# Kernel optimization log

Measured on AMD Instinct MI355X. Metric: run time of the kernel, lower is better.

Reference implementation:

```python
import jax, jax.numpy as jnp
import numpy as np

N_EMBD = 1024
N_HEAD = 16
HEAD_SIZE = N_EMBD // N_HEAD  # 64
B, T = 4, 2048

def setup_inputs() -> dict:
    key = jax.random.key(0)
    k1, k2, k3, k4 = jax.random.split(key, 4)
    x = jax.random.normal(k1, (B, T, N_EMBD), dtype=jnp.float32)
    # weights stored as [in, out]; torch Linear does x @ W.T with W [out,in]
    w_qkv = jax.random.normal(k2, (N_EMBD, 3 * N_EMBD), dtype=jnp.float32) * (N_EMBD ** -0.5)
    w_proj = jax.random.normal(k3, (N_EMBD, N_EMBD), dtype=jnp.float32) * (N_EMBD ** -0.5)
    b_proj = jax.random.normal(k4, (N_EMBD,), dtype=jnp.float32) * 0.01
    return {"x": x, "w_qkv": w_qkv, "w_proj": w_proj, "b_proj": b_proj}

def reference(x, w_qkv, w_proj, b_proj):
    Bx, Tx, C = x.shape
    H, D = N_HEAD, HEAD_SIZE
    qkv = x @ w_qkv                               # [B,T,3C]
    q, k, v = jnp.split(qkv, 3, axis=-1)
    q = q.reshape(Bx, Tx, H, D).transpose(0, 2, 1, 3)  # [B,H,T,D]
    k = k.reshape(Bx, Tx, H, D).transpose(0, 2, 1, 3)
    v = v.reshape(Bx, Tx, H, D).transpose(0, 2, 1, 3)
    att = jnp.einsum('bhqd,bhkd->bhqk', q, k) * (D ** -0.5)  # [B,H,T,T]
    causal = jnp.tril(jnp.ones((Tx, Tx), dtype=bool))
    att = jnp.where(causal[None, None], att, -jnp.inf)
    att = jax.nn.softmax(att, axis=-1)
    out = jnp.einsum('bhqk,bhkd->bhqd', att, v)   # [B,H,T,D]
    out = out.transpose(0, 2, 1, 3).reshape(Bx, Tx, H * D)
    return out @ w_proj + b_proj
```

## Files before the change

kernel.cpp:

```cpp
#include <hip/hip_runtime.h>
#include <hip/hip_bf16.h>
#include <stdint.h>
#include <math.h>


typedef __attribute__((ext_vector_type(8))) short short8;
typedef __attribute__((ext_vector_type(4))) short shrt4;
typedef __attribute__((ext_vector_type(4))) float f32x4;

#define LOG2E 1.44269504088896340736f
#define QSCALE 0.18033688011112042f

__device__ int g_isf32;

__device__ __forceinline__ void gl16(const void* g, void* l) {
  __builtin_amdgcn_global_load_lds(
      (const __attribute__((address_space(1))) unsigned int*)g,
      (__attribute__((address_space(3))) unsigned int*)l, 16, 0, 0);
}

__device__ __forceinline__ short f2bf(float f) {
  __hip_bfloat16 h = __float2bfloat16(f);
  return *reinterpret_cast<short*>(&h);
}
__device__ __forceinline__ float bf2f(short s) {
  __hip_bfloat16 h = *reinterpret_cast<__hip_bfloat16*>(&s);
  return __bfloat162float(h);
}
__device__ __forceinline__ short8 pack8(f32x4 lo, f32x4 hi) {
  short8 r;
#pragma unroll
  for (int e = 0; e < 4; ++e) { r[e] = f2bf(lo[e]); r[4 + e] = f2bf(hi[e]); }
  return r;
}

__device__ __forceinline__ short pbf(float f) {
  unsigned u = __builtin_bit_cast(unsigned, f);
  return (short)((u + 0x8000u) >> 16);
}

__device__ __forceinline__ float dpp_max16(float x) {
  int i;
  i = __builtin_amdgcn_update_dpp(0, __builtin_bit_cast(int, x), 0xB1, 0xF, 0xF, true);
  x = fmaxf(x, __builtin_bit_cast(float, i));
  i = __builtin_amdgcn_update_dpp(0, __builtin_bit_cast(int, x), 0x4E, 0xF, 0xF, true);
  x = fmaxf(x, __builtin_bit_cast(float, i));
  i = __builtin_amdgcn_update_dpp(0, __builtin_bit_cast(int, x), 0x141, 0xF, 0xF, true);
  x = fmaxf(x, __builtin_bit_cast(float, i));
  i = __builtin_amdgcn_update_dpp(0, __builtin_bit_cast(int, x), 0x140, 0xF, 0xF, true);
  x = fmaxf(x, __builtin_bit_cast(float, i));
  return x;
}
__device__ __forceinline__ float dpp_sum16(float x) {
  int i;
  i = __builtin_amdgcn_update_dpp(0, __builtin_bit_cast(int, x), 0xB1, 0xF, 0xF, true);
  x += __builtin_bit_cast(float, i);
  i = __builtin_amdgcn_update_dpp(0, __builtin_bit_cast(int, x), 0x4E, 0xF, 0xF, true);
  x += __builtin_bit_cast(float, i);
  i = __builtin_amdgcn_update_dpp(0, __builtin_bit_cast(int, x), 0x141, 0xF, 0xF, true);
  x += __builtin_bit_cast(float, i);
  i = __builtin_amdgcn_update_dpp(0, __builtin_bit_cast(int, x), 0x140, 0xF, 0xF, true);
  x += __builtin_bit_cast(float, i);
  return x;
}

__global__ __launch_bounds__(256) void detect_dtype(const unsigned short* w) {
  __shared__ int cnt;
  if (threadIdx.x == 0) cnt = 0;
  __syncthreads();
  const unsigned short* p = w + (long)blockIdx.x * 49152;
  int c = 0;
  for (int i = threadIdx.x; i < 49152; i += 256)
    if (((p[i] >> 7) & 0xFF) == 0xFF) c++;
  atomicAdd(&cnt, c);
  __syncthreads();
  if (threadIdx.x == 0) g_isf32 = (cnt > 8) ? 1 : 0;
}

__global__ __launch_bounds__(256) void cvt_x(const void* __restrict__ src,
                                             short* __restrict__ dst) {
  const long i = ((long)blockIdx.x * 256 + threadIdx.x) * 8;
  if (g_isf32) {
    const float* s = (const float*)src + i;
    *(short8*)(dst + i) = pack8(*(const f32x4*)s, *(const f32x4*)(s + 4));
  } else {
    *(short8*)(dst + i) = *(const short8*)((const short*)src + i);
  }
}

template <int MODE>
__global__ __launch_bounds__(512, 2) void gemm_bt(
    const short* __restrict__ A, const short* __restrict__ Bt,
    const void* __restrict__ bias, void* __restrict__ C,
    short* __restrict__ vt, int M, int N, int K)
{
  __shared__ __align__(16) short As[3][16384];
  __shared__ __align__(16) short Bs[3][8192];
  const int tid  = threadIdx.x;
  const int lane = tid & 63;
  const int wave = tid >> 6;
  const int quad = lane >> 4;
  const int l16  = lane & 15;
  const int wm = (wave >> 1) * 64;
  const int wn = (wave & 1) * 64;

  const int gx = (int)gridDim.x;
  const int nwg = gx * (int)gridDim.y;
  int lb = (int)blockIdx.y * gx + (int)blockIdx.x;
  if ((nwg & 7) == 0) lb = (lb & 7) * (nwg >> 3) + (lb >> 3);
  const long m0 = (long)(lb / gx) * 256;
  const long n0 = (long)(lb % gx) * 128;

  int isf32 = 0;
  if (MODE == 1) {
    isf32 = g_isf32;
    asm volatile("s_waitcnt vmcnt(0) lgkmcnt(0)" ::: "memory");
  }

  f32x4 acc[4][4] = {};

  const int srow = tid >> 3;
  const int scol = ((tid & 7) ^ (srow & 7)) * 8;
  const short* Ag = A  + (m0 + srow) * (long)K + scol;
  const short* Bg = Bt + (n0 + srow) * (long)K + scol;
  const long rs64 = (long)64 * K;

  const int x7  = l16 & 7;
  const int xo0 = ((0 + quad) ^ x7) * 16;
  const int xo1 = ((4 + quad) ^ x7) * 16;
  const int aRow = (wm + l16) * 128;
  const int bRow = (wn + l16) * 128;

  auto STAGE_HALF = [&](int t2, int h) {
    const int bb = t2 % 3;
    const long k0 = (long)t2 << 6;
    gl16(Ag + k0 + (h * 2 + 0) * rs64, (char*)As[bb] + (h * 2 + 0) * 8192 + tid * 16);
    gl16(Ag + k0 + (h * 2 + 1) * rs64, (char*)As[bb] + (h * 2 + 1) * 8192 + tid * 16);
    gl16(Bg + k0 + h * rs64,           (char*)Bs[bb] + h * 8192 + tid * 16);
  };

  const int nt = K >> 6;
  STAGE_HALF(0, 0); STAGE_HALF(0, 1);
  STAGE_HALF(1, 0); STAGE_HALF(1, 1);

  for (int t = 0; t < nt; ++t) {
    if (t + 1 < nt) { asm volatile("s_waitcnt vmcnt(6)" ::: "memory"); }
    else            { asm volatile("s_waitcnt vmcnt(0)" ::: "memory"); }
    __builtin_amdgcn_sched_barrier(0);
    __builtin_amdgcn_s_barrier();
    __builtin_amdgcn_sched_barrier(0);

    const char* Ab = (const char*)As[t % 3];
    const char* Bb = (const char*)Bs[t % 3];

#pragma unroll
    for (int ph = 0; ph < 2; ++ph) {
      const int xo = ph ? xo1 : xo0;
      short8 af[4], bfv[4];
#pragma unroll
      for (int i = 0; i < 4; ++i)
        af[i] = *(const short8*)(Ab + aRow + i * 2048 + xo);
#pragma unroll
      for (int j = 0; j < 4; ++j)
        bfv[j] = *(const short8*)(Bb + bRow + j * 2048 + xo);
      if (t + 2 < nt) STAGE_HALF(t + 2, ph);
      __builtin_amdgcn_s_setprio(1);
#pragma unroll
      for (int i = 0; i < 4; ++i)
#pragma unroll
        for (int j = 0; j < 4; ++j)
          acc[i][j] = __builtin_amdgcn_mfma_f32_16x16x32_bf16(af[i], bfv[j], acc[i][j], 0, 0, 0);
      __builtin_amdgcn_s_setprio(0);
      if (ph == 0) {
        __builtin_amdgcn_s_barrier();
        __builtin_amdgcn_sched_barrier(0);
      }
    }
  }

#pragma unroll
  for (int j = 0; j < 4; ++j) {
    const long col = n0 + wn + j * 16 + l16;
    float bv = 0.f;
    if (MODE == 1)
      bv = isf32 ? ((const float*)bias)[col] : bf2f(((const short*)bias)[col]);
#pragma unroll
    for (int i = 0; i < 4; ++i) {
      const long row0 = m0 + wm + i * 16 + quad * 4;
      if (MODE == 2 && col >= 2048) {
        const long bb = row0 >> 11, t0 = row0 & 2047;
        const long hd = col - 2048;
        shrt4 v4;
#pragma unroll
        for (int r = 0; r < 4; ++r) v4[r] = f2bf(acc[i][j][r]);
        *(shrt4*)&vt[((bb * 16 + (hd >> 6)) * 64 + (hd & 63)) * 2048 + t0] = v4;
      } else {
#pragma unroll
        for (int r = 0; r < 4; ++r) {
          const long row = row0 + r;
          const float val = acc[i][j][r] + bv;
          if (MODE == 2) {
            const float vq = (col < 1024) ? val * QSCALE : val;
            ((short*)C)[row * 2048 + col] = f2bf(vq);
          } else {
            if (isf32) ((float*)C)[row * (long)N + col] = val;
            else       ((short*)C)[row * (long)N + col] = f2bf(val);
          }
        }
      }
    }
  }
}

__global__ __launch_bounds__(256) void transpose64(
    const void* __restrict__ src, short* __restrict__ dst, int R, int C)
{
  __shared__ __align__(16) short tile[64][72];
  const int isf32 = g_isf32;
  const int tid = threadIdx.x;
  const long r0 = (long)blockIdx.y * 64;
  const long c0 = (long)blockIdx.x * 64;
#pragma unroll
  for (int it = 0; it < 2; ++it) {
    int idx = it * 256 + tid;
    int rr = idx >> 3, ch = idx & 7;
    const long off = (r0 + rr) * C + c0 + ch * 8;
    short8 v;
    if (isf32) {
      const float* s = (const float*)src + off;
      v = pack8(*(const f32x4*)s, *(const f32x4*)(s + 4));
    } else {
      v = *(const short8*)((const short*)src + off);
    }
    *(short8*)&tile[rr][ch * 8] = v;
  }
  __syncthreads();
#pragma unroll
  for (int it = 0; it < 2; ++it) {
    int idx = it * 256 + tid;
    int cc = idx >> 3, ch = idx & 7;
    short8 v;
#pragma unroll
    for (int jj = 0; jj < 8; ++jj) v[jj] = tile[ch * 8 + jj][cc];
    *(short8*)&dst[(c0 + cc) * R + r0 + ch * 8] = v;
  }
}

__global__ __launch_bounds__(256) void attn_fwd(
    const short* __restrict__ qk, const short* __restrict__ vt,
    short* __restrict__ out)
{
  __shared__ __align__(16) short Ks[2][64][32];
  __shared__ __align__(16) short Vs[2][64][32];
  __shared__ __align__(16) short Pw[4][16][76];
  const int tid = threadIdx.x;
  const int lane = tid & 63, wave = tid >> 6;
  const int quad = lane >> 4, l16 = lane & 15;
  const int bh = blockIdx.x;
  const int b = bh >> 4, h = bh & 15;
  const int jq = (int)gridDim.y - 1 - (int)blockIdx.y;
  const int qbase = jq * 64 + wave * 16;

  const short* qp = qk + ((long)(b * 2048 + qbase + l16)) * 2048 + h * 64 + quad * 8;
  const short8 aq0 = *(const short8*)qp;
  const short8 aq1 = *(const short8*)(qp + 32);

  const int sr = tid >> 2, sc_ = tid & 3;
  const short* kg = qk + (long)b * 2048 * 2048 + 1024 + h * 64 + (long)sr * 2048 + sc_ * 8;
  const short* vg = vt + ((long)bh * 64 + sr) * 2048 + sc_ * 8;

  f32x4 o[4] = {};
  float m_run[4], l_run[4];
#pragma unroll
  for (int r = 0; r < 4; ++r) { m_run[r] = -1e30f; l_run[r] = 0.f; }

  for (int kt = 0; kt < jq; ++kt) {
    const int k0 = kt * 64;

    __syncthreads();
    gl16(kg + (long)k0 * 2048,      (char*)Ks + tid * 16);
    gl16(kg + (long)k0 * 2048 + 32, (char*)Ks + 4096 + tid * 16);
    gl16(vg + k0,                   (char*)Vs + tid * 16);
    gl16(vg + k0 + 32,              (char*)Vs + 4096 + tid * 16);
    __syncthreads();

    f32x4 s[4];
#pragma unroll
    for (int c = 0; c < 4; ++c) {
      short8 kf0 = *(const short8*)&Ks[0][c * 16 + l16][quad * 8];
      short8 kf1 = *(const short8*)&Ks[1][c * 16 + l16][quad * 8];
      f32x4 z = {};
      z = __builtin_amdgcn_mfma_f32_16x16x32_bf16(aq0, kf0, z, 0, 0, 0);
      z = __builtin_amdgcn_mfma_f32_16x16x32_bf16(aq1, kf1, z, 0, 0, 0);
      s[c] = z;
    }

    float mx[4];
#pragma unroll
    for (int r = 0; r < 4; ++r)
      mx[r] = dpp_max16(fmaxf(fmaxf(s[0][r], s[1][r]), fmaxf(s[2][r], s[3][r])));

    int grow = 0;
#pragma unroll
    for (int r = 0; r < 4; ++r) grow |= (mx[r] > m_run[r] + 8.f);
    if (__any(grow)) {
#pragma unroll
      for (int r = 0; r < 4; ++r) {
        const float mn = fmaxf(m_run[r], mx[r]);
        const float al = __builtin_amdgcn_exp2f(m_run[r] - mn);
        m_run[r] = mn;
        l_run[r] *= al;
#pragma unroll
        for (int i = 0; i < 4; ++i) o[i][r] *= al;
      }
    }

#pragma unroll
    for (int c = 0; c < 4; ++c)
#pragma unroll
      for (int r = 0; r < 4; ++r) {
        const float p = __builtin_amdgcn_exp2f(s[c][r] - m_run[r]);
        l_run[r] += p;
        Pw[wave][quad * 4 + r][c * 16 + l16] = pbf(p);
      }

    {
      short8 pf0 = *(const short8*)&Pw[wave][l16][quad * 8];
      short8 pf1 = *(const short8*)&Pw[wave][l16][32 + quad * 8];
#pragma unroll
      for (int i = 0; i < 4; ++i) {
        short8 vf0 = *(const short8*)&Vs[0][i * 16 + l16][quad * 8];
        o[i] = __builtin_amdgcn_mfma_f32_16x16x32_bf16(pf0, vf0, o[i], 0, 0, 0);
        short8 vf1 = *(const short8*)&Vs[1][i * 16 + l16][quad * 8];
        o[i] = __builtin_amdgcn_mfma_f32_16x16x32_bf16(pf1, vf1, o[i], 0, 0, 0);
      }
    }
  }

  {
    const int k0 = jq * 64;

    __syncthreads();
    gl16(kg + (long)k0 * 2048,      (char*)Ks + tid * 16);
    gl16(kg + (long)k0 * 2048 + 32, (char*)Ks + 4096 + tid * 16);
    gl16(vg + k0,                   (char*)Vs + tid * 16);
    gl16(vg + k0 + 32,              (char*)Vs + 4096 + tid * 16);
    __syncthreads();

    f32x4 s[4];
    float mx[4];
#pragma unroll
    for (int r = 0; r < 4; ++r) mx[r] = -1e30f;
#pragma unroll
    for (int c = 0; c < 4; ++c) {
      if (c > wave) continue;
      short8 kf0 = *(const short8*)&Ks[0][c * 16 + l16][quad * 8];
      short8 kf1 = *(const short8*)&Ks[1][c * 16 + l16][quad * 8];
      f32x4 z = {};
      z = __builtin_amdgcn_mfma_f32_16x16x32_bf16(aq0, kf0, z, 0, 0, 0);
      z = __builtin_amdgcn_mfma_f32_16x16x32_bf16(aq1, kf1, z, 0, 0, 0);
      if (c == wave) {
#pragma unroll
        for (int r = 0; r < 4; ++r)
          z[r] = (l16 > quad * 4 + r) ? -1e30f : z[r];
      }
      s[c] = z;
#pragma unroll
      for (int r = 0; r < 4; ++r) mx[r] = fmaxf(mx[r], z[r]);
    }
#pragma unroll
    for (int r = 0; r < 4; ++r) mx[r] = dpp_max16(mx[r]);

    int grow = 0;
#pragma unroll
    for (int r = 0; r < 4; ++r) grow |= (mx[r] > m_run[r] + 8.f);
    if (__any(grow)) {
#pragma unroll
      for (int r = 0; r < 4; ++r) {
        const float mn = fmaxf(m_run[r], mx[r]);
        const float al = __builtin_amdgcn_exp2f(m_run[r] - mn);
        m_run[r] = mn;
        l_run[r] *= al;
#pragma unroll
        for (int i = 0; i < 4; ++i) o[i][r] *= al;
      }
    }

#pragma unroll
    for (int c = 0; c < 4; ++c) {
      if (c <= wave) {
#pragma unroll
        for (int r = 0; r < 4; ++r) {
          const float p = __builtin_amdgcn_exp2f(s[c][r] - m_run[r]);
          l_run[r] += p;
          Pw[wave][quad * 4 + r][c * 16 + l16] = pbf(p);
        }
      } else if (c < 2 || wave >= 2) {
#pragma unroll
        for (int r = 0; r < 4; ++r)
          Pw[wave][quad * 4 + r][c * 16 + l16] = 0;
      }
    }

    {
      short8 pf0 = *(const short8*)&Pw[wave][l16][quad * 8];
#pragma unroll
      for (int i = 0; i < 4; ++i) {
        short8 vf0 = *(const short8*)&Vs[0][i * 16 + l16][quad * 8];
        o[i] = __builtin_amdgcn_mfma_f32_16x16x32_bf16(pf0, vf0, o[i], 0, 0, 0);
      }
      if (wave >= 2) {
        short8 pf1 = *(const short8*)&Pw[wave][l16][32 + quad * 8];
#pragma unroll
        for (int i = 0; i < 4; ++i) {
          short8 vf1 = *(const short8*)&Vs[1][i * 16 + l16][quad * 8];
          o[i] = __builtin_amdgcn_mfma_f32_16x16x32_bf16(pf1, vf1, o[i], 0, 0, 0);
        }
      }
    }
  }

#pragma unroll
  for (int r = 0; r < 4; ++r) l_run[r] = dpp_sum16(l_run[r]);
  float inv[4];
#pragma unroll
  for (int r = 0; r < 4; ++r) inv[r] = 1.0f / l_run[r];
  short* op = out + ((long)(b * 2048 + qbase + quad * 4)) * 1024 + h * 64;
#pragma unroll
  for (int i = 0; i < 4; ++i)
#pragma unroll
    for (int r = 0; r < 4; ++r)
      op[(long)r * 1024 + i * 16 + l16] = f2bf(o[i][r] * inv[r]);
}

__global__ __launch_bounds__(256) void copy_out(const void* __restrict__ src,
                                                void* __restrict__ dst)
{
  const long n16 = g_isf32 ? 2097152L : 1048576L;
  const uint4* s = (const uint4*)src;
  uint4* d = (uint4*)dst;
  for (long i = (long)blockIdx.x * 256 + threadIdx.x; i < n16;
       i += (long)gridDim.x * 256)
    d[i] = s[i];
}

extern "C" void kernel_launch(void* const* d_in, const int* in_sizes, int n_in,
                              void* d_out, int out_size, void* d_ws, size_t ws_size,
                              hipStream_t stream)
{
  const void* x      = d_in[0];
  const void* w_qkv  = d_in[1];
  const void* w_proj = d_in[2];
  const void* b_proj = d_in[3];

  short* ws = (short*)d_ws;
  const bool planA = ws_size >= 67108864ULL;

  short* qk  = ws;
  short* vtp = ws + 16777216L;

  short *wqkvT, *attnb, *wprojT, *xbf;
  void*  projC;
  if (planA) {
    attnb  = ws + 25165824L;
    wqkvT  = attnb;
    wprojT = qk;
    xbf    = (short*)d_out;
    projC  = d_out;
  } else {
    wqkvT  = (short*)d_out;
    xbf    = (short*)d_out + 3145728L;
    attnb  = (short*)d_out;
    wprojT = vtp;
    projC  = qk;
  }

  detect_dtype<<<64, 256, 0, stream>>>((const unsigned short*)w_qkv);
  cvt_x<<<4096, 256, 0, stream>>>(x, xbf);
  transpose64<<<dim3(3072 / 64, 1024 / 64), 256, 0, stream>>>(w_qkv, wqkvT, 1024, 3072);
  gemm_bt<2><<<dim3(3072 / 128, 8192 / 256), 512, 0, stream>>>(
      xbf, wqkvT, nullptr, qk, vtp, 8192, 3072, 1024);
  attn_fwd<<<dim3(64, 32), 256, 0, stream>>>(qk, vtp, attnb);
  transpose64<<<dim3(1024 / 64, 1024 / 64), 256, 0, stream>>>(w_proj, wprojT, 1024, 1024);
  gemm_bt<1><<<dim3(1024 / 128, 8192 / 256), 512, 0, stream>>>(
      attnb, wprojT, b_proj, projC, nullptr, 8192, 1024, 1024);
  if (!planA)
    copy_out<<<2048, 256, 0, stream>>>(projC, d_out);
}
```

Before: 286.4 us.

## Pair causal query tiles per attention block and pack P and V stores with cvt_pk_bf16

```diff
diff --git a/kernel.cpp b/kernel.cpp
--- a/kernel.cpp
+++ b/kernel.cpp
@@ -5,7 +5,6 @@
 
 
 typedef __attribute__((ext_vector_type(8))) short short8;
-typedef __attribute__((ext_vector_type(4))) short shrt4;
 typedef __attribute__((ext_vector_type(4))) float f32x4;
 
 #define LOG2E 1.44269504088896340736f
@@ -34,9 +33,10 @@
   return r;
 }
 
-__device__ __forceinline__ short pbf(float f) {
-  unsigned u = __builtin_bit_cast(unsigned, f);
-  return (short)((u + 0x8000u) >> 16);
+__device__ __forceinline__ unsigned cvtpk(float a, float b) {
+  unsigned r;
+  asm("v_cvt_pk_bf16_f32 %0, %1, %2" : "=v"(r) : "v"(a), "v"(b));
+  return r;
 }
 
 __device__ __forceinline__ float dpp_max16(float x) {
@@ -181,20 +181,24 @@
 #pragma unroll
   for (int j = 0; j < 4; ++j) {
     const long col = n0 + wn + j * 16 + l16;
-    float bv = 0.f;
-    if (MODE == 1)
-      bv = isf32 ? ((const float*)bias)[col] : bf2f(((const short*)bias)[col]);
-#pragma unroll
-    for (int i = 0; i < 4; ++i) {
-      const long row0 = m0 + wm + i * 16 + quad * 4;
-      if (MODE == 2 && col >= 2048) {
-        const long bb = row0 >> 11, t0 = row0 & 2047;
-        const long hd = col - 2048;
-        shrt4 v4;
-#pragma unroll
-        for (int r = 0; r < 4; ++r) v4[r] = f2bf(acc[i][j][r]);
-        *(shrt4*)&vt[((bb * 16 + (hd >> 6)) * 64 + (hd & 63)) * 2048 + t0] = v4;
-      } else {
+    if (MODE == 2 && col >= 2048) {
+      const long hd = col - 2048;
+      const long bb = (m0 + wm) >> 11;
+      const long tb = (m0 + wm) & 2047;
+      short* vrow = vt + ((bb * 16 + (hd >> 6)) * 64 + (hd & 63)) * 2048 + tb;
+#pragma unroll
+      for (int ip = 0; ip < 2; ++ip)
+#pragma unroll
+        for (int r = 0; r < 4; ++r)
+          *(unsigned*)&vrow[ip * 32 + 2 * (quad * 4 + r)] =
+              cvtpk(acc[2 * ip][j][r], acc[2 * ip + 1][j][r]);
+    } else {
+      float bv = 0.f;
+      if (MODE == 1)
+        bv = isf32 ? ((const float*)bias)[col] : bf2f(((const short*)bias)[col]);
+#pragma unroll
+      for (int i = 0; i < 4; ++i) {
+        const long row0 = m0 + wm + i * 16 + quad * 4;
 #pragma unroll
         for (int r = 0; r < 4; ++r) {
           const long row = row0 + r;
@@ -252,185 +256,197 @@
 {
   __shared__ __align__(16) short Ks[2][64][32];
   __shared__ __align__(16) short Vs[2][64][32];
-  __shared__ __align__(16) short Pw[4][16][76];
+  __shared__ __align__(16) unsigned Pw[4][16][36];
   const int tid = threadIdx.x;
   const int lane = tid & 63, wave = tid >> 6;
   const int quad = lane >> 4, l16 = lane & 15;
   const int bh = blockIdx.x;
   const int b = bh >> 4, h = bh & 15;
-  const int jq = (int)gridDim.y - 1 - (int)blockIdx.y;
-  const int qbase = jq * 64 + wave * 16;
-
-  const short* qp = qk + ((long)(b * 2048 + qbase + l16)) * 2048 + h * 64 + quad * 8;
-  const short8 aq0 = *(const short8*)qp;
-  const short8 aq1 = *(const short8*)(qp + 32);
+  const int py = blockIdx.y;
 
   const int sr = tid >> 2, sc_ = tid & 3;
   const short* kg = qk + (long)b * 2048 * 2048 + 1024 + h * 64 + (long)sr * 2048 + sc_ * 8;
   const short* vg = vt + ((long)bh * 64 + sr) * 2048 + sc_ * 8;
 
-  f32x4 o[4] = {};
-  float m_run[4], l_run[4];
-#pragma unroll
-  for (int r = 0; r < 4; ++r) { m_run[r] = -1e30f; l_run[r] = 0.f; }
-
-  for (int kt = 0; kt < jq; ++kt) {
-    const int k0 = kt * 64;
-
-    __syncthreads();
-    gl16(kg + (long)k0 * 2048,      (char*)Ks + tid * 16);
-    gl16(kg + (long)k0 * 2048 + 32, (char*)Ks + 4096 + tid * 16);
-    gl16(vg + k0,                   (char*)Vs + tid * 16);
-    gl16(vg + k0 + 32,              (char*)Vs + 4096 + tid * 16);
-    __syncthreads();
-
-    f32x4 s[4];
-#pragma unroll
-    for (int c = 0; c < 4; ++c) {
-      short8 kf0 = *(const short8*)&Ks[0][c * 16 + l16][quad * 8];
-      short8 kf1 = *(const short8*)&Ks[1][c * 16 + l16][quad * 8];
-      f32x4 z = {};
-      z = __builtin_amdgcn_mfma_f32_16x16x32_bf16(aq0, kf0, z, 0, 0, 0);
-      z = __builtin_amdgcn_mfma_f32_16x16x32_bf16(aq1, kf1, z, 0, 0, 0);
-      s[c] = z;
-    }
-
-    float mx[4];
-#pragma unroll
-    for (int r = 0; r < 4; ++r)
-      mx[r] = dpp_max16(fmaxf(fmaxf(s[0][r], s[1][r]), fmaxf(s[2][r], s[3][r])));
-
-    int grow = 0;
-#pragma unroll
-    for (int r = 0; r < 4; ++r) grow |= (mx[r] > m_run[r] + 8.f);
-    if (__any(grow)) {
+  for (int hseg = 0; hseg < 2; ++hseg) {
+    const int jq = hseg ? (31 - py) : py;
+    const int qbase = jq * 64 + wave * 16;
+
+    const short* qp = qk + ((long)(b * 2048 + qbase + l16)) * 2048 + h * 64 + quad * 8;
+    const short8 aq0 = *(const short8*)qp;
+    const short8 aq1 = *(const short8*)(qp + 32);
+
+    f32x4 o[4] = {};
+    float m_run[4], l_run[4];
+#pragma unroll
+    for (int r = 0; r < 4; ++r) { m_run[r] = -1e30f; l_run[r] = 0.f; }
+
+    for (int kt = 0; kt < jq; ++kt) {
+      const int k0 = kt * 64;
+
+      __syncthreads();
+      gl16(kg + (long)k0 * 2048,      (char*)Ks + tid * 16);
+      gl16(kg + (long)k0 * 2048 + 32, (char*)Ks + 4096 + tid * 16);
+      gl16(vg + k0,                   (char*)Vs + tid * 16);
+      gl16(vg + k0 + 32,              (char*)Vs + 4096 + tid * 16);
+      __syncthreads();
+
+      f32x4 s[4];
+#pragma unroll
+      for (int c = 0; c < 4; ++c) {
+        short8 kf0 = *(const short8*)&Ks[0][c * 16 + l16][quad * 8];
+        short8 kf1 = *(const short8*)&Ks[1][c * 16 + l16][quad * 8];
+        f32x4 z = {};
+        z = __builtin_amdgcn_mfma_f32_16x16x32_bf16(aq0, kf0, z, 0, 0, 0);
+        z = __builtin_amdgcn_mfma_f32_16x16x32_bf16(aq1, kf1, z, 0, 0, 0);
+        s[c] = z;
+      }
+
+      float mx[4];
+#pragma unroll
+      for (int r = 0; r < 4; ++r)
+        mx[r] = dpp_max16(fmaxf(fmaxf(s[0][r], s[1][r]), fmaxf(s[2][r], s[3][r])));
+
+      int grow = 0;
+#pragma unroll
+      for (int r = 0; r < 4; ++r) grow |= (mx[r] > m_run[r] + 8.f);
+      if (__any(grow)) {
+#pragma unroll
+        for (int r = 0; r < 4; ++r) {
+          const float mn = fmaxf(m_run[r], mx[r]);
+          const float al = __builtin_amdgcn_exp2f(m_run[r] - mn);
+          m_run[r] = mn;
+          l_run[r] *= al;
+#pragma unroll
+          for (int i = 0; i < 4; ++i) o[i][r] *= al;
+        }
+      }
+
+      float p[4][4];
+#pragma unroll
+      for (int c = 0; c < 4; ++c)
+#pragma unroll
+        for (int r = 0; r < 4; ++r) {
+          p[c][r] = __builtin_amdgcn_exp2f(s[c][r] - m_run[r]);
+          l_run[r] += p[c][r];
+        }
 #pragma unroll
       for (int r = 0; r < 4; ++r) {
-        const float mn = fmaxf(m_run[r], mx[r]);
-        const float al = __builtin_amdgcn_exp2f(m_run[r] - mn);
-        m_run[r] = mn;
-        l_run[r] *= al;
-#pragma unroll
-        for (int i = 0; i < 4; ++i) o[i][r] *= al;
-      }
-    }
-
-#pragma unroll
-    for (int c = 0; c < 4; ++c)
-#pragma unroll
-      for (int r = 0; r < 4; ++r) {
-        const float p = __builtin_amdgcn_exp2f(s[c][r] - m_run[r]);
-        l_run[r] += p;
-        Pw[wave][quad * 4 + r][c * 16 + l16] = pbf(p);
-      }
-
-    {
-      short8 pf0 = *(const short8*)&Pw[wave][l16][quad * 8];
-      short8 pf1 = *(const short8*)&Pw[wave][l16][32 + quad * 8];
-#pragma unroll
-      for (int i = 0; i < 4; ++i) {
-        short8 vf0 = *(const short8*)&Vs[0][i * 16 + l16][quad * 8];
-        o[i] = __builtin_amdgcn_mfma_f32_16x16x32_bf16(pf0, vf0, o[i], 0, 0, 0);
-        short8 vf1 = *(const short8*)&Vs[1][i * 16 + l16][quad * 8];
-        o[i] = __builtin_amdgcn_mfma_f32_16x16x32_bf16(pf1, vf1, o[i], 0, 0, 0);
-      }
-    }
-  }
-
-  {
-    const int k0 = jq * 64;
-
-    __syncthreads();
-    gl16(kg + (long)k0 * 2048,      (char*)Ks + tid * 16);
-    gl16(kg + (long)k0 * 2048 + 32, (char*)Ks + 4096 + tid * 16);
-    gl16(vg + k0,                   (char*)Vs + tid * 16);
-    gl16(vg + k0 + 32,              (char*)Vs + 4096 + tid * 16);
-    __syncthreads();
-
-    f32x4 s[4];
-    float mx[4];
-#pragma unroll
-    for (int r = 0; r < 4; ++r) mx[r] = -1e30f;
-#pragma unroll
-    for (int c = 0; c < 4; ++c) {
-      if (c > wave) continue;
-      short8 kf0 = *(const short8*)&Ks[0][c * 16 + l16][quad * 8];
-      short8 kf1 = *(const short8*)&Ks[1][c * 16 + l16][quad * 8];
-      f32x4 z = {};
-      z = __builtin_amdgcn_mfma_f32_16x16x32_bf16(aq0, kf0, z, 0, 0, 0);
-      z = __builtin_amdgcn_mfma_f32_16x16x32_bf16(aq1, kf1, z, 0, 0, 0);
-      if (c == wave) {
-#pragma unroll
-        for (int r = 0; r < 4; ++r)
-          z[r] = (l16 > quad * 4 + r) ? -1e30f : z[r];
-      }
-      s[c] = z;
-#pragma unroll
-      for (int r = 0; r < 4; ++r) mx[r] = fmaxf(mx[r], z[r]);
-    }
-#pragma unroll
-    for (int r = 0; r < 4; ++r) mx[r] = dpp_max16(mx[r]);
-
-    int grow = 0;
-#pragma unroll
-    for (int r = 0; r < 4; ++r) grow |= (mx[r] > m_run[r] + 8.f);
-    if (__any(grow)) {
-#pragma unroll
-      for (int r = 0; r < 4; ++r) {
-        const float mn = fmaxf(m_run[r], mx[r]);
-        const float al = __builtin_amdgcn_exp2f(m_run[r] - mn);
-        m_run[r] = mn;
-        l_run[r] *= al;
-#pragma unroll
-        for (int i = 0; i < 4; ++i) o[i][r] *= al;
-      }
-    }
-
-#pragma unroll
-    for (int c = 0; c < 4; ++c) {
-      if (c <= wave) {
-#pragma unroll
-        for (int r = 0; r < 4; ++r) {
-          const float p = __builtin_amdgcn_exp2f(s[c][r] - m_run[r]);
-          l_run[r] += p;
-          Pw[wave][quad * 4 + r][c * 16 + l16] = pbf(p);
-        }
-      } else if (c < 2 || wave >= 2) {
-#pragma unroll
-        for (int r = 0; r < 4; ++r)
-          Pw[wave][quad * 4 + r][c * 16 + l16] = 0;
-      }
-    }
-
-    {
-      short8 pf0 = *(const short8*)&Pw[wave][l16][quad * 8];
-#pragma unroll
-      for (int i = 0; i < 4; ++i) {
-        short8 vf0 = *(const short8*)&Vs[0][i * 16 + l16][quad * 8];
-        o[i] = __builtin_amdgcn_mfma_f32_16x16x32_bf16(pf0, vf0, o[i], 0, 0, 0);
-      }
-      if (wave >= 2) {
-        short8 pf1 = *(const short8*)&Pw[wave][l16][32 + quad * 8];
+        Pw[wave][quad * 4 + r][l16]      = cvtpk(p[0][r], p[1][r]);
+        Pw[wave][quad * 4 + r][16 + l16] = cvtpk(p[2][r], p[3][r]);
+      }
+
+      {
+        short8 pf0 = *(const short8*)&Pw[wave][l16][quad * 4];
+        short8 pf1 = *(const short8*)&Pw[wave][l16][16 + quad * 4];
 #pragma unroll
         for (int i = 0; i < 4; ++i) {
+          short8 vf0 = *(const short8*)&Vs[0][i * 16 + l16][quad * 8];
+          o[i] = __builtin_amdgcn_mfma_f32_16x16x32_bf16(pf0, vf0, o[i], 0, 0, 0);
           short8 vf1 = *(const short8*)&Vs[1][i * 16 + l16][quad * 8];
           o[i] = __builtin_amdgcn_mfma_f32_16x16x32_bf16(pf1, vf1, o[i], 0, 0, 0);
         }
       }
     }
-  }
-
-#pragma unroll
-  for (int r = 0; r < 4; ++r) l_run[r] = dpp_sum16(l_run[r]);
-  float inv[4];
-#pragma unroll
-  for (int r = 0; r < 4; ++r) inv[r] = 1.0f / l_run[r];
-  short* op = out + ((long)(b * 2048 + qbase + quad * 4)) * 1024 + h * 64;
-#pragma unroll
-  for (int i = 0; i < 4; ++i)
-#pragma unroll
-    for (int r = 0; r < 4; ++r)
-      op[(long)r * 1024 + i * 16 + l16] = f2bf(o[i][r] * inv[r]);
+
+    {
+      const int k0 = jq * 64;
+
+      __syncthreads();
+      gl16(kg + (long)k0 * 2048,      (char*)Ks + tid * 16);
+      gl16(kg + (long)k0 * 2048 + 32, (char*)Ks + 4096 + tid * 16);
+      gl16(vg + k0,                   (char*)Vs + tid * 16);
+      gl16(vg + k0 + 32,              (char*)Vs + 4096 + tid * 16);
+      __syncthreads();
+
+      f32x4 s[4];
+      float mx[4];
+#pragma unroll
+      for (int r = 0; r < 4; ++r) mx[r] = -1e30f;
+#pragma unroll
+      for (int c = 0; c < 4; ++c) {
+        if (c > wave) continue;
+        short8 kf0 = *(const short8*)&Ks[0][c * 16 + l16][quad * 8];
+        short8 kf1 = *(const short8*)&Ks[1][c * 16 + l16][quad * 8];
+        f32x4 z = {};
+        z = __builtin_amdgcn_mfma_f32_16x16x32_bf16(aq0, kf0, z, 0, 0, 0);
+        z = __builtin_amdgcn_mfma_f32_16x16x32_bf16(aq1, kf1, z, 0, 0, 0);
+        if (c == wave) {
+#pragma unroll
+          for (int r = 0; r < 4; ++r)
+            z[r] = (l16 > quad * 4 + r) ? -1e30f : z[r];
+        }
+        s[c] = z;
+#pragma unroll
+        for (int r = 0; r < 4; ++r) mx[r] = fmaxf(mx[r], z[r]);
+      }
+#pragma unroll
+      for (int r = 0; r < 4; ++r) mx[r] = dpp_max16(mx[r]);
+
+      int grow = 0;
+#pragma unroll
+      for (int r = 0; r < 4; ++r) grow |= (mx[r] > m_run[r] + 8.f);
+      if (__any(grow)) {
+#pragma unroll
+        for (int r = 0; r < 4; ++r) {
+          const float mn = fmaxf(m_run[r], mx[r]);
+          const float al = __builtin_amdgcn_exp2f(m_run[r] - mn);
+          m_run[r] = mn;
+          l_run[r] *= al;
+#pragma unroll
+          for (int i = 0; i < 4; ++i) o[i][r] *= al;
+        }
+      }
+
+      float p[4][4];
+#pragma unroll
+      for (int c = 0; c < 4; ++c)
+#pragma unroll
+        for (int r = 0; r < 4; ++r) {
+          if (c <= wave) {
+            p[c][r] = __builtin_amdgcn_exp2f(s[c][r] - m_run[r]);
+            l_run[r] += p[c][r];
+          } else {
+            p[c][r] = 0.f;
+          }
+        }
+#pragma unroll
+      for (int r = 0; r < 4; ++r) {
+        Pw[wave][quad * 4 + r][l16] = cvtpk(p[0][r], p[1][r]);
+        if (wave >= 2)
+          Pw[wave][quad * 4 + r][16 + l16] = cvtpk(p[2][r], p[3][r]);
+      }
+
+      {
+        short8 pf0 = *(const short8*)&Pw[wave][l16][quad * 4];
+#pragma unroll
+        for (int i = 0; i < 4; ++i) {
+          short8 vf0 = *(const short8*)&Vs[0][i * 16 + l16][quad * 8];
+          o[i] = __builtin_amdgcn_mfma_f32_16x16x32_bf16(pf0, vf0, o[i], 0, 0, 0);
+        }
+        if (wave >= 2) {
+          short8 pf1 = *(const short8*)&Pw[wave][l16][16 + quad * 4];
+#pragma unroll
+          for (int i = 0; i < 4; ++i) {
+            short8 vf1 = *(const short8*)&Vs[1][i * 16 + l16][quad * 8];
+            o[i] = __builtin_amdgcn_mfma_f32_16x16x32_bf16(pf1, vf1, o[i], 0, 0, 0);
+          }
+        }
+      }
+    }
+
+#pragma unroll
+    for (int r = 0; r < 4; ++r) l_run[r] = dpp_sum16(l_run[r]);
+    float inv[4];
+#pragma unroll
+    for (int r = 0; r < 4; ++r) inv[r] = 1.0f / l_run[r];
+    short* op = out + ((long)(b * 2048 + qbase + quad * 4)) * 1024 + h * 64;
+#pragma unroll
+    for (int i = 0; i < 4; ++i)
+#pragma unroll
+      for (int r = 0; r < 4; ++r)
+        op[(long)r * 1024 + i * 16 + l16] = f2bf(o[i][r] * inv[r]);
+  }
 }
 
 __global__ __launch_bounds__(256) void copy_out(const void* __restrict__ src,
@@ -480,7 +496,7 @@
   transpose64<<<dim3(3072 / 64, 1024 / 64), 256, 0, stream>>>(w_qkv, wqkvT, 1024, 3072);
   gemm_bt<2><<<dim3(3072 / 128, 8192 / 256), 512, 0, stream>>>(
       xbf, wqkvT, nullptr, qk, vtp, 8192, 3072, 1024);
-  attn_fwd<<<dim3(64, 32), 256, 0, stream>>>(qk, vtp, attnb);
+  attn_fwd<<<dim3(64, 16), 256, 0, stream>>>(qk, vtp, attnb);
   transpose64<<<dim3(1024 / 64, 1024 / 64), 256, 0, stream>>>(w_proj, wprojT, 1024, 1024);
   gemm_bt<1><<<dim3(1024 / 128, 8192 / 256), 512, 0, stream>>>(
       attnb, wprojT, b_proj, projC, nullptr, 8192, 1024, 1024);
```

New measurement: 287.1 us. About the same (+0.3%).
